# Optimization experiments

Hardware: AMD Instinct MI355X
Metric: run time of the kernel (lower is better)

Reference implementation:

```python
import jax, jax.numpy as jnp
import numpy as np

B, A_IN, C_IN, H, W_ = 8, 16, 4, 64, 64   # batch, input atoms, input capsules, spatial
K, C_OUT, A_OUT, ROUTINGS = 5, 8, 32, 3
EPS = 1e-7


def setup_inputs() -> dict:
    key = jax.random.key(0)
    k1, k2 = jax.random.split(key)
    x = jax.random.normal(k1, (B, A_IN, C_IN, H, W_), dtype=jnp.float32)
    # kaiming_uniform_(fan_in, relu): bound = sqrt(3) * sqrt(2) / sqrt(fan_in)
    fan_in = A_IN * K * K
    bound = float(np.sqrt(6.0 / fan_in))
    W = jax.random.uniform(k2, (C_OUT * A_OUT, A_IN, K, K), jnp.float32, -bound, bound)
    b = jnp.full((1, 1, C_OUT, A_OUT), 0.1, dtype=jnp.float32)
    return {"x": x, "W": W, "b": b}


def _squash(v):
    # v: (..., atoms); SegCaps squash with epsilon inside sqrt
    sq = jnp.sum(v * v, axis=-1, keepdims=True)
    return v * (sq / (1.0 + sq) / jnp.sqrt(sq + EPS))


def reference(x, W, b):
    # Faithful to torch: permute then raw row-major reshapes (byte reinterpret)
    t = jnp.transpose(x, (2, 0, 3, 4, 1))                      # (C_IN, B, H, W, A_IN)
    t = t.reshape(C_IN * B, H, W_, A_IN).reshape(-1, A_IN, H, W_)
    conv = jax.lax.conv_general_dilated(
        t, W, window_strides=(1, 1), padding="SAME",
        dimension_numbers=("NCHW", "OIHW", "NCHW"))             # (C_IN*B, C_OUT*A_OUT, h, w)
    ch, cw = conv.shape[2], conv.shape[3]
    votes = conv.reshape(B, C_IN, ch, cw, C_OUT, A_OUT)         # raw reinterpret, as in torch
    biases = jnp.tile(b, (ch, cw, 1, 1))                        # (h, w, C_OUT, A_OUT)

    # dynamic routing (SegCaps update_routing)
    logits = jnp.zeros((B, C_IN, ch, cw, C_OUT), dtype=votes.dtype)
    activation = None
    for _ in range(ROUTINGS):
        route = jax.nn.softmax(logits, axis=-1)                 # (B, Cin, h, w, Cout)
        preact = jnp.einsum("bihwo,bihwoa->bhwoa", route, votes) + biases
        activation = _squash(preact)                            # (B, h, w, Cout, A)
        agreement = jnp.einsum("bihwoa,bhwoa->bihwo", votes, activation)
        logits = logits + agreement
    return jnp.transpose(activation, (0, 4, 3, 1, 2))           # (B, A_OUT, C_OUT, h, w)
```

## Files before the change

kernel.cpp:

```cpp
#include <hip/hip_runtime.h>
#include <hip/hip_bf16.h>


typedef _Float16 half8 __attribute__((ext_vector_type(8)));
typedef _Float16 half4v __attribute__((ext_vector_type(4)));
typedef float floatx4 __attribute__((ext_vector_type(4)));
typedef unsigned uint2v __attribute__((ext_vector_type(2)));

#define EPSF 1e-7f

template <int CTRL>
__device__ __forceinline__ float dppmov(float x) {
  return __int_as_float(__builtin_amdgcn_update_dpp(
      0, __float_as_int(x), CTRL, 0xf, 0xf, false));
}
__device__ __forceinline__ float red_g_add(float x) {
  x += dppmov<0xB1>(x);
  x += dppmov<0x4E>(x);
  return x;
}
__device__ __forceinline__ float red_o2_add(float x) {
  x += dppmov<0x124>(x);
  x += dppmov<0x128>(x);
  uint2v r = __builtin_amdgcn_permlane16_swap(
      __float_as_uint(x), __float_as_uint(x), false, false);
  return __uint_as_float(r[0]) + __uint_as_float(r[1]);
}
__device__ __forceinline__ float red_o2_max(float x) {
  x = fmaxf(x, dppmov<0x124>(x));
  x = fmaxf(x, dppmov<0x128>(x));
  uint2v r = __builtin_amdgcn_permlane16_swap(
      __float_as_uint(x), __float_as_uint(x), false, false);
  return fmaxf(__uint_as_float(r[0]), __uint_as_float(r[1]));
}

__global__ __launch_bounds__(1024) void k_pack_all(const float* __restrict__ x,
                                                   const float* __restrict__ W,
                                                   _Float16* __restrict__ th,
                                                   _Float16* __restrict__ Wp) {
  __shared__ float lin[32 * 306 + 18];
  const int bid = blockIdx.x;
  const int tid = threadIdx.x;

  if (bid >= 256) {
    int id = (bid - 256) * 1024 + tid;
    int a  = id & 15;
    int oc = (id >> 4) & 255;
    int kk = id >> 12;
    Wp[id] = (kk < 25) ? (_Float16)W[oc * 400 + a * 25 + kk] : (_Float16)0.0f;
    return;
  }

  const int n   = bid >> 3;
  const int a0h = (bid >> 2) & 1;
  const int W0  = (bid & 3) * 16;
  const int ci = n >> 3, b0 = n & 7;
  const float* xb = x + b0 * 262144 + ci * 4096 + W0;

  for (int p = 0; p < 2; ++p) {
    int rr = p * 256 + (tid >> 2);
    int q  = (tid & 3) * 4;
    int a1 = rr >> 5, m = rr & 31;
    float4 v = *(const float4*)(xb + a1 * 16384 + (a0h * 32 + m) * 64 + q);
    float* d = lin + m * 306 + a1 * 18 + q;
    d[0] = v.x; d[1] = v.y; d[2] = v.z; d[3] = v.w;
  }
  __syncthreads();

  _Float16* tb = th + (size_t)n * 65536 + a0h * 32768 + W0 * 128;
  {
    int hh = tid >> 8;
    int w1 = (tid >> 4) & 15;
    int a1 = tid & 15;
    half8 v;
#pragma unroll
    for (int j = 0; j < 8; ++j)
      v[j] = (_Float16)lin[(j * 4 + hh) * 306 + a1 * 18 + w1];
    *(half8*)(tb + hh * 8192 + w1 * 128 + a1 * 8) = v;
  }
}

__global__ __launch_bounds__(512) void k_conv(const _Float16* __restrict__ th,
                                              const _Float16* __restrict__ Wp,
                                              _Float16* __restrict__ votes) {
  __shared__ _Float16 lds[16384];
  const int orig = blockIdx.x;
  const int lid  = (orig & 7) * 256 + (orig >> 3);
  const int y = lid & 63;
  const int n = lid >> 6;
  const int tid = threadIdx.x;

  for (int c = tid; c < 680; c += 512) {
    int a0h = c / 340;
    int rem = c - a0h * 340;
    int r   = rem / 68;
    int col = rem - r * 68;
    int row = y + r - 2;
    half8 v = {};
    if (col >= 2 && col <= 65 && row >= 0 && row < 64)
      v = *(const half8*)(th + (size_t)(((n * 2 + a0h) * 64 + row) * 64 + (col - 2)) * 8);
    *(half8*)(lds + c * 8) = v;
  }
  __syncthreads();

  const int lane  = tid & 63;
  const int wv    = tid >> 6;
  const int col16 = lane & 15;
  const int quad  = lane >> 4;
  const int t     = quad >> 1;
  const int a0h   = quad & 1;
  const int m0    = wv * 32;

  floatx4 acc[2][4] = {};

  const _Float16* wbase = Wp + (size_t)t * 4096 + (m0 + col16) * 16 + a0h * 8;
  const _Float16* lbase = lds + (a0h * 340 + col16) * 8;

  half8 bfc[4], awc[2], bfn[4], awn[2];
  {
    const _Float16* lb = lbase + (t ? 1 : 0) * 8;
#pragma unroll
    for (int xt = 0; xt < 4; ++xt)
      bfc[xt] = *(const half8*)(lb + xt * 128);
#pragma unroll
    for (int oct = 0; oct < 2; ++oct)
      awc[oct] = *(const half8*)(wbase + oct * 256);
  }

#pragma unroll
  for (int s = 0; s < 13; ++s) {
    if (s < 12) {
      const int k0 = 2 * (s + 1);
      const int k1 = (2 * (s + 1) + 1 > 24) ? 24 : 2 * (s + 1) + 1;
      const int e0 = (k0 / 5) * 68 + (k0 % 5);
      const int e1 = (k1 / 5) * 68 + (k1 % 5);
      const _Float16* lb = lbase + (t ? e1 : e0) * 8;
#pragma unroll
      for (int xt = 0; xt < 4; ++xt)
        bfn[xt] = *(const half8*)(lb + xt * 128);
#pragma unroll
      for (int oct = 0; oct < 2; ++oct)
        awn[oct] = *(const half8*)(wbase + (size_t)(s + 1) * 8192 + oct * 256);
    }
#pragma unroll
    for (int oct = 0; oct < 2; ++oct)
#pragma unroll
      for (int xt = 0; xt < 4; ++xt)
        acc[oct][xt] = __builtin_amdgcn_mfma_f32_16x16x32_f16(
            awc[oct], bfc[xt], acc[oct][xt], 0, 0, 0);
    if (s < 12) {
#pragma unroll
      for (int xt = 0; xt < 4; ++xt) bfc[xt] = bfn[xt];
#pragma unroll
      for (int oct = 0; oct < 2; ++oct) awc[oct] = awn[oct];
    }
  }

  __syncthreads();
#pragma unroll
  for (int oct = 0; oct < 2; ++oct)
#pragma unroll
    for (int xt = 0; xt < 4; ++xt)
#pragma unroll
      for (int r = 0; r < 4; ++r) {
        int oc = m0 + oct * 16 + quad * 4 + r;
        int xx = xt * 16 + col16;
        int sw = (oc & 15) >> 1;
        lds[oc * 64 + (xx ^ (sw << 3))] = (_Float16)acc[oct][xt][r];
      }
  __syncthreads();
  _Float16* vb2 = votes + (size_t)n * 1048576 + y * 64;
#pragma unroll
  for (int it = 0; it < 4; ++it) {
    int idx = it * 512 + tid;
    int oc  = idx >> 3;
    int x0  = (idx & 7) << 3;
    int sw  = (oc & 15) >> 1;
    half8 hv = *(const half8*)(lds + oc * 64 + (x0 ^ (sw << 3)));
    *(half8*)(vb2 + (size_t)oc * 4096 + x0) = hv;
  }
}

__global__ __launch_bounds__(256) void k_routing9(
    const _Float16* __restrict__ votes, const float* __restrict__ bias,
    float* __restrict__ out) {
  __shared__ float so[256 * 9];
  const int tid  = threadIdx.x;
  const int lane = tid & 63;
  const int wv   = tid >> 6;
  const int bid  = blockIdx.x;
  const int bv = bid >> 9;
  const int h  = (bid >> 3) & 63;
  const int W0 = (bid & 7) * 8;

  const int half = lane >> 5;
  const int o    = (lane >> 2) & 7;
  const int g    = lane & 3;
  const int col  = wv * 2 + half;
  const int w    = W0 + col;

  float bb[8];
  {
    const float4 b0 = *(const float4*)(bias + o * 32 + g * 8);
    const float4 b1 = *(const float4*)(bias + o * 32 + g * 8 + 4);
    bb[0]=b0.x; bb[1]=b0.y; bb[2]=b0.z; bb[3]=b0.w;
    bb[4]=b1.x; bb[5]=b1.y; bb[6]=b1.z; bb[7]=b1.w;
  }

  const _Float16* vb = votes + (size_t)bv * 4194304 + h * 16384 + w * 256
                     + o * 32 + g * 8;
  float v[4][8];
#pragma unroll
  for (int i = 0; i < 4; ++i) {
    half8 hv = *(const half8*)(vb + (size_t)i * 1048576);
#pragma unroll
    for (int j = 0; j < 8; ++j) v[i][j] = (float)hv[j];
  }

  float logit[4], act[8], pr[8];

#pragma unroll
  for (int j = 0; j < 8; ++j)
    pr[j] = fmaf(0.125f, (v[0][j] + v[1][j]) + (v[2][j] + v[3][j]), bb[j]);
  {
    float sq = pr[0]*pr[0];
#pragma unroll
    for (int j = 1; j < 8; ++j) sq = fmaf(pr[j], pr[j], sq);
    sq = red_g_add(sq);
    float sc = sq * __builtin_amdgcn_rcpf(1.f + sq)
                  * __builtin_amdgcn_rsqf(sq + EPSF);
#pragma unroll
    for (int j = 0; j < 8; ++j) act[j] = pr[j] * sc;
  }
#pragma unroll
  for (int i = 0; i < 4; ++i) {
    float ag = v[i][0] * act[0];
#pragma unroll
    for (int j = 1; j < 8; ++j) ag = fmaf(v[i][j], act[j], ag);
    logit[i] = red_g_add(ag);
  }

#pragma unroll
  for (int r = 1; r < 3; ++r) {
    float route[4];
#pragma unroll
    for (int i = 0; i < 4; ++i) {
      float m = red_o2_max(logit[i]);
      float e = __expf(logit[i] - m);
      float s = red_o2_add(e);
      route[i] = e * __builtin_amdgcn_rcpf(s);
    }
#pragma unroll
    for (int j = 0; j < 8; ++j) pr[j] = bb[j];
#pragma unroll
    for (int i = 0; i < 4; ++i)
#pragma unroll
      for (int j = 0; j < 8; ++j)
        pr[j] = fmaf(route[i], v[i][j], pr[j]);
    float sq = pr[0]*pr[0];
#pragma unroll
    for (int j = 1; j < 8; ++j) sq = fmaf(pr[j], pr[j], sq);
    sq = red_g_add(sq);
    float sc = sq * __builtin_amdgcn_rcpf(1.f + sq)
                  * __builtin_amdgcn_rsqf(sq + EPSF);
#pragma unroll
    for (int j = 0; j < 8; ++j) act[j] = pr[j] * sc;
    if (r < 2) {
#pragma unroll
      for (int i = 0; i < 4; ++i) {
        float ag = v[i][0] * act[0];
#pragma unroll
        for (int j = 1; j < 8; ++j) ag = fmaf(v[i][j], act[j], ag);
        logit[i] += red_g_add(ag);
      }
    }
  }

#pragma unroll
  for (int j = 0; j < 8; ++j)
    so[(g * 64 + j * 8 + o) * 9 + (col ^ g)] = act[j];
  __syncthreads();

  float* ob = out + (size_t)bv * 1048576 + h * 64 + W0;
#pragma unroll
  for (int p = 0; p < 4; ++p) {
    int r  = p * 64 + (tid >> 2);
    int c2 = (tid & 3) * 2;
    float lo = so[r * 9 + (c2 ^ p)];
    float hi = so[r * 9 + ((c2 + 1) ^ p)];
    *(float2*)(ob + (size_t)r * 4096 + c2) = make_float2(lo, hi);
  }
}

extern "C" void kernel_launch(void* const* d_in, const int* in_sizes, int n_in,
                              void* d_out, int out_size, void* d_ws, size_t ws_size,
                              hipStream_t stream) {
  const float* x  = (const float*)d_in[0];
  const float* W  = (const float*)d_in[1];
  const float* b  = (const float*)d_in[2];
  float* out = (float*)d_out;

  _Float16* th    = (_Float16*)d_ws;
  _Float16* Wp    = th + 2097152;
  _Float16* votes = Wp + 106496;

  k_pack_all<<<360, 1024, 0, stream>>>(x, W, th, Wp);
  k_conv<<<2048, 512, 0, stream>>>(th, Wp, votes);
  k_routing9<<<4096, 256, 0, stream>>>(votes, b, out);
}
```

Baseline: 127.3 us.

## Compute two output rows per conv block to reuse the input halo tile

Each conv block now produces two adjacent output rows instead of one. It loads a 6-row halo tile and runs two accumulator sets that share the same LDS B-fragments, with the second row's weights offset by one kernel row. This halves the grid and reduces redundant halo loads and B-fragment LDS reads per output. In exchange each thread holds twice the accumulators, which raises register pressure; the launch-bounds hint of 4 blocks may cap registers. The epilogue writes the two rows out in two passes.

```diff
diff --git a/kernel.cpp b/kernel.cpp
--- a/kernel.cpp
+++ b/kernel.cpp
@@ -80,22 +80,23 @@
   }
 }
 
-__global__ __launch_bounds__(512) void k_conv(const _Float16* __restrict__ th,
-                                              const _Float16* __restrict__ Wp,
-                                              _Float16* __restrict__ votes) {
+__global__ __launch_bounds__(512, 4) void k_conv(const _Float16* __restrict__ th,
+                                                 const _Float16* __restrict__ Wp,
+                                                 _Float16* __restrict__ votes) {
   __shared__ _Float16 lds[16384];
   const int orig = blockIdx.x;
-  const int lid  = (orig & 7) * 256 + (orig >> 3);
-  const int y = lid & 63;
-  const int n = lid >> 6;
+  const int lid  = (orig & 7) * 128 + (orig >> 3);
+  const int ypair = lid & 31;
+  const int n     = lid >> 5;
+  const int y0    = ypair * 2;
   const int tid = threadIdx.x;
 
-  for (int c = tid; c < 680; c += 512) {
-    int a0h = c / 340;
-    int rem = c - a0h * 340;
+  for (int c = tid; c < 816; c += 512) {
+    int a0h = c / 408;
+    int rem = c - a0h * 408;
     int r   = rem / 68;
     int col = rem - r * 68;
-    int row = y + r - 2;
+    int row = y0 + r - 2;
     half8 v = {};
     if (col >= 2 && col <= 65 && row >= 0 && row < 64)
       v = *(const half8*)(th + (size_t)(((n * 2 + a0h) * 64 + row) * 64 + (col - 2)) * 8);
@@ -111,73 +112,91 @@
   const int a0h   = quad & 1;
   const int m0    = wv * 32;
 
-  floatx4 acc[2][4] = {};
-
-  const _Float16* wbase = Wp + (size_t)t * 4096 + (m0 + col16) * 16 + a0h * 8;
-  const _Float16* lbase = lds + (a0h * 340 + col16) * 8;
-
-  half8 bfc[4], awc[2], bfn[4], awn[2];
+  floatx4 accA[2][4] = {}, accB[2][4] = {};
+
+  const int wrest = (m0 + col16) * 16 + a0h * 8;
+  const _Float16* wbase = Wp + t * 4096 + wrest;
+  const _Float16* lbase = lds + (a0h * 408 + col16) * 8;
+
+  half8 bfc[4], bfn[4];
   {
     const _Float16* lb = lbase + (t ? 1 : 0) * 8;
 #pragma unroll
     for (int xt = 0; xt < 4; ++xt)
       bfc[xt] = *(const half8*)(lb + xt * 128);
-#pragma unroll
-    for (int oct = 0; oct < 2; ++oct)
-      awc[oct] = *(const half8*)(wbase + oct * 256);
-  }
-
-#pragma unroll
-  for (int s = 0; s < 13; ++s) {
-    if (s < 12) {
-      const int k0 = 2 * (s + 1);
-      const int k1 = (2 * (s + 1) + 1 > 24) ? 24 : 2 * (s + 1) + 1;
-      const int e0 = (k0 / 5) * 68 + (k0 % 5);
-      const int e1 = (k1 / 5) * 68 + (k1 % 5);
-      const _Float16* lb = lbase + (t ? e1 : e0) * 8;
+  }
+
+#pragma unroll
+  for (int s = 0; s < 15; ++s) {
+    if (s < 14) {
+      const int kn0 = 2 * (s + 1);
+      const int kn1 = 2 * (s + 1) + 1;
+      const int offn0 = (kn0 / 5) * 68 + (kn0 % 5);
+      const int offn1 = (kn1 / 5) * 68 + (kn1 % 5);
+      const _Float16* lb = lbase + (t ? offn1 : offn0) * 8;
 #pragma unroll
       for (int xt = 0; xt < 4; ++xt)
         bfn[xt] = *(const half8*)(lb + xt * 128);
+    }
+    if (s <= 12) {
+      half8 awA[2];
 #pragma unroll
       for (int oct = 0; oct < 2; ++oct)
-        awn[oct] = *(const half8*)(wbase + (size_t)(s + 1) * 8192 + oct * 256);
-    }
+        awA[oct] = *(const half8*)(wbase + (size_t)s * 8192 + oct * 256);
+#pragma unroll
+      for (int oct = 0; oct < 2; ++oct)
+#pragma unroll
+        for (int xt = 0; xt < 4; ++xt)
+          accA[oct][xt] = __builtin_amdgcn_mfma_f32_16x16x32_f16(
+              awA[oct], bfc[xt], accA[oct][xt], 0, 0, 0);
+    }
+    if (s >= 2) {
+      const _Float16* wb = (s == 2)
+          ? (Wp + (t ? 0 : 25 * 4096) + wrest)
+          : (wbase + (size_t)(s - 2) * 8192 - 4096);
+      half8 awB[2];
+#pragma unroll
+      for (int oct = 0; oct < 2; ++oct)
+        awB[oct] = *(const half8*)(wb + oct * 256);
+#pragma unroll
+      for (int oct = 0; oct < 2; ++oct)
+#pragma unroll
+        for (int xt = 0; xt < 4; ++xt)
+          accB[oct][xt] = __builtin_amdgcn_mfma_f32_16x16x32_f16(
+              awB[oct], bfc[xt], accB[oct][xt], 0, 0, 0);
+    }
+    if (s < 14) {
+#pragma unroll
+      for (int xt = 0; xt < 4; ++xt) bfc[xt] = bfn[xt];
+    }
+  }
+
+#pragma unroll
+  for (int pass = 0; pass < 2; ++pass) {
+    const floatx4 (&acc)[2][4] = pass ? accB : accA;
+    __syncthreads();
 #pragma unroll
     for (int oct = 0; oct < 2; ++oct)
 #pragma unroll
       for (int xt = 0; xt < 4; ++xt)
-        acc[oct][xt] = __builtin_amdgcn_mfma_f32_16x16x32_f16(
-            awc[oct], bfc[xt], acc[oct][xt], 0, 0, 0);
-    if (s < 12) {
-#pragma unroll
-      for (int xt = 0; xt < 4; ++xt) bfc[xt] = bfn[xt];
-#pragma unroll
-      for (int oct = 0; oct < 2; ++oct) awc[oct] = awn[oct];
-    }
-  }
-
-  __syncthreads();
-#pragma unroll
-  for (int oct = 0; oct < 2; ++oct)
-#pragma unroll
-    for (int xt = 0; xt < 4; ++xt)
-#pragma unroll
-      for (int r = 0; r < 4; ++r) {
-        int oc = m0 + oct * 16 + quad * 4 + r;
-        int xx = xt * 16 + col16;
-        int sw = (oc & 15) >> 1;
-        lds[oc * 64 + (xx ^ (sw << 3))] = (_Float16)acc[oct][xt][r];
-      }
-  __syncthreads();
-  _Float16* vb2 = votes + (size_t)n * 1048576 + y * 64;
-#pragma unroll
-  for (int it = 0; it < 4; ++it) {
-    int idx = it * 512 + tid;
-    int oc  = idx >> 3;
-    int x0  = (idx & 7) << 3;
-    int sw  = (oc & 15) >> 1;
-    half8 hv = *(const half8*)(lds + oc * 64 + (x0 ^ (sw << 3)));
-    *(half8*)(vb2 + (size_t)oc * 4096 + x0) = hv;
+#pragma unroll
+        for (int r = 0; r < 4; ++r) {
+          int oc = m0 + oct * 16 + quad * 4 + r;
+          int xx = xt * 16 + col16;
+          int sw = (oc & 15) >> 1;
+          lds[oc * 64 + (xx ^ (sw << 3))] = (_Float16)acc[oct][xt][r];
+        }
+    __syncthreads();
+    _Float16* vb2 = votes + (size_t)n * 1048576 + (y0 + pass) * 64;
+#pragma unroll
+    for (int it = 0; it < 4; ++it) {
+      int idx = it * 512 + tid;
+      int oc  = idx >> 3;
+      int x0  = (idx & 7) << 3;
+      int sw  = (oc & 15) >> 1;
+      half8 hv = *(const half8*)(lds + oc * 64 + (x0 ^ (sw << 3)));
+      *(half8*)(vb2 + (size_t)oc * 4096 + x0) = hv;
+    }
   }
 }
 
@@ -305,6 +324,6 @@
   _Float16* votes = Wp + 106496;
 
   k_pack_all<<<360, 1024, 0, stream>>>(x, W, th, Wp);
-  k_conv<<<2048, 512, 0, stream>>>(th, Wp, votes);
+  k_conv<<<1024, 512, 0, stream>>>(th, Wp, votes);
   k_routing9<<<4096, 256, 0, stream>>>(votes, b, out);
 }
```

Result: no change. 128.3 us (+0.7%).
